# Kernel tuning notes

Measured on AMD Instinct MI355X. Metric: run time of the kernel, lower is better.

The kernel has to match this reference:

```python
import jax, jax.numpy as jnp
import numpy as np

VOCAB = 128
HID = 1024
B = 128
T = 512


def setup_inputs() -> dict:
    key = jax.random.key(0)
    ks = jax.random.split(key, 5)
    x = jax.random.randint(ks[0], (B, T), 0, VOCAB)
    Wxh = jax.random.normal(ks[1], (VOCAB, HID), dtype=jnp.float32) * 0.01
    Whh = jax.random.normal(ks[2], (HID, HID), dtype=jnp.float32) * 0.01
    bh = jnp.zeros((HID,), dtype=jnp.float32)
    # nn.Linear(hidden*2, vocab): weight [vocab, 2*hidden], bias [vocab]
    fc_w = jax.random.normal(ks[3], (VOCAB, 2 * HID), dtype=jnp.float32) * 0.02
    fc_b = jnp.zeros((VOCAB,), dtype=jnp.float32)
    return {"x": x, "Wxh": Wxh, "Whh": Whh, "bh": bh, "fc_w": fc_w, "fc_b": fc_b}


def reference(x, Wxh, Whh, bh, fc_w, fc_b):
    # one_hot(x) @ Wxh  ==  row gather from Wxh
    xe = Wxh[x]  # [B, T, H]
    h0 = jnp.zeros((x.shape[0], Whh.shape[0]), dtype=xe.dtype)

    def step(h, xt):
        h = jnp.tanh(xt + h @ Whh + bh)
        return h, h

    _, Hs = jax.lax.scan(step, h0, jnp.swapaxes(xe, 0, 1))  # [T, B, H]
    Hs = jnp.swapaxes(Hs, 0, 1)  # [B, T, H]

    # per-step full (non-causal) self-attention over hidden states, batched over t
    scores = jnp.einsum("bth,bsh->bts", Hs, Hs)          # [B, T, T]
    weights = jax.nn.softmax(scores, axis=-1)
    context = jnp.einsum("bts,bsh->bth", weights, Hs)     # [B, T, H]

    combined = jnp.concatenate([Hs, context], axis=-1)    # [B, T, 2H]
    outputs = combined @ fc_w.T + fc_b                    # [B, T, V]
    return outputs
```

## Files before the change

### kernel.cpp

```cpp
#include <hip/hip_runtime.h>
#include <cmath>

#define HID 1024
#define NB  128
#define NT  512
#define NV  128
#define NBLK 256

using u16 = unsigned short;
using u32 = unsigned int;

typedef __attribute__((ext_vector_type(8))) short s16x8;
typedef __attribute__((ext_vector_type(4))) float f32x4;

static __device__ __forceinline__ float bf2f(u16 u) {
  union { u32 i; float f; } v; v.i = ((u32)u) << 16; return v.f;
}
static __device__ __forceinline__ u16 f2bf(float f) {
  union { u32 i; float f; } v; v.f = f;
  u32 r = v.i + 0x7FFFu + ((v.i >> 16) & 1u);
  return (u16)(r >> 16);
}

__global__ __launch_bounds__(128, 1) void rnn_persist(
    const int* __restrict__ x, const float* __restrict__ Wxh,
    const float* __restrict__ Whh, const float* __restrict__ bh,
    u16* __restrict__ Hs, u32* __restrict__ ctr)
{
  const int blk  = blockIdx.x;
  const int bg   = blk & 7;
  const int cg   = blk >> 3;
  const int tid  = threadIdx.x;
  const int wave = tid >> 6;
  const int lane = tid & 63;
  const int b0   = bg * 16;
  const int c0   = cg * 32;

  __shared__ u16 Wt[32 * 1024];
  __shared__ __align__(16) u16 hstage[16 * 1024];

  for (int it = 0; it < 128; ++it) {
    int idx = tid + it * 128;
    int col = idx & 31;
    int k   = (idx >> 5) * 2;
    float w0 = Whh[(size_t)k * HID + c0 + col];
    float w1 = Whh[(size_t)(k + 1) * HID + c0 + col];
    u32 pk = ((u32)f2bf(w1) << 16) | (u32)f2bf(w0);
    u32 byteo = ((u32)col * 2048 + (u32)k * 2) ^ ((u32)(col & 7) << 4);
    *reinterpret_cast<u32*>(reinterpret_cast<char*>(Wt) + byteo) = pk;
  }

  const int frow = lane & 15;
  const int koff = (lane >> 4) * 8;
  const int col  = wave * 16 + (lane & 15);
  const int cc   = c0 + col;
  const u32 swz   = (u32)(col & 7) << 4;
  const u32 bbase = (u32)col * 2048 + (u32)koff * 2;
  const char* wtb = reinterpret_cast<const char*>(Wt);
  const char* hsb = reinterpret_cast<const char*>(hstage);
  const u32 abase = (u32)frow * 2048 + (u32)koff * 2;
  const u32 axor  = (u32)(frow & 7) << 4;

  const int srow = tid >> 3;
  const int scol = tid & 7;
  const u32 sxor = (u32)(srow & 7) << 4;
  char* sdst = reinterpret_cast<char*>(hstage) + (u32)srow * 2048;

  const float bhv = bh[cc];
  float xr[4];
  #pragma unroll
  for (int r = 0; r < 4; ++r) {
    int m = (lane >> 4) * 4 + r;
    int xt = x[(size_t)(b0 + m) * NT];
    xr[r] = Wxh[(size_t)xt * HID + cc] + bhv;
  }
  __syncthreads();

  u32* __restrict__ myctr = ctr + bg * 64;

  for (int t = 0; t < NT; ++t) {
    if (t > 0) {
      const char* src = reinterpret_cast<const char*>(
          Hs + ((size_t)(b0 + srow) * NT + (t - 1)) * HID) + scol * 16;
      uint4 s[16];
      asm volatile(
        "global_load_dwordx4 %0, %16, off sc0 sc1\n\t"
        "global_load_dwordx4 %1, %16, off offset:128 sc0 sc1\n\t"
        "global_load_dwordx4 %2, %16, off offset:256 sc0 sc1\n\t"
        "global_load_dwordx4 %3, %16, off offset:384 sc0 sc1\n\t"
        "global_load_dwordx4 %4, %16, off offset:512 sc0 sc1\n\t"
        "global_load_dwordx4 %5, %16, off offset:640 sc0 sc1\n\t"
        "global_load_dwordx4 %6, %16, off offset:768 sc0 sc1\n\t"
        "global_load_dwordx4 %7, %16, off offset:896 sc0 sc1\n\t"
        "global_load_dwordx4 %8, %16, off offset:1024 sc0 sc1\n\t"
        "global_load_dwordx4 %9, %16, off offset:1152 sc0 sc1\n\t"
        "global_load_dwordx4 %10, %16, off offset:1280 sc0 sc1\n\t"
        "global_load_dwordx4 %11, %16, off offset:1408 sc0 sc1\n\t"
        "global_load_dwordx4 %12, %16, off offset:1536 sc0 sc1\n\t"
        "global_load_dwordx4 %13, %16, off offset:1664 sc0 sc1\n\t"
        "global_load_dwordx4 %14, %16, off offset:1792 sc0 sc1\n\t"
        "global_load_dwordx4 %15, %16, off offset:1920 sc0 sc1\n\t"
        "s_waitcnt vmcnt(0)"
        : "=&v"(s[0]), "=&v"(s[1]), "=&v"(s[2]), "=&v"(s[3]),
          "=&v"(s[4]), "=&v"(s[5]), "=&v"(s[6]), "=&v"(s[7]),
          "=&v"(s[8]), "=&v"(s[9]), "=&v"(s[10]), "=&v"(s[11]),
          "=&v"(s[12]), "=&v"(s[13]), "=&v"(s[14]), "=&v"(s[15])
        : "v"(src) : "memory");
      __builtin_amdgcn_sched_barrier(0);
      #pragma unroll
      for (int j = 0; j < 16; ++j)
        *reinterpret_cast<uint4*>(sdst +
            (((u32)(scol * 16 + j * 128)) ^ sxor)) = s[j];
    }
    __syncthreads();

    f32x4 acc = {0.f, 0.f, 0.f, 0.f};
    if (t > 0) {
      #pragma unroll 8
      for (int kc = 0; kc < 32; ++kc) {
        s16x8 af = *reinterpret_cast<const s16x8*>(hsb + ((abase + (u32)kc * 64) ^ axor));
        s16x8 bf = *reinterpret_cast<const s16x8*>(wtb + ((bbase + (u32)kc * 64) ^ swz));
        acc = __builtin_amdgcn_mfma_f32_16x16x32_bf16(af, bf, acc, 0, 0, 0);
      }
    }

    #pragma unroll
    for (int r = 0; r < 4; ++r) {
      int m = (lane >> 4) * 4 + r;
      float h = tanhf(acc[r] + xr[r]);
      u16 hb = f2bf(h);
      u16* pa = Hs + ((size_t)(b0 + m) * NT + t) * HID + cc;
      asm volatile("global_store_short %0, %1, off sc0 sc1"
                   :: "v"(pa), "v"((u32)hb) : "memory");
    }
    asm volatile("s_waitcnt vmcnt(0)" ::: "memory");
    __syncthreads();

    if (tid == 0 && t < NT - 1)
      __hip_atomic_fetch_add(myctr, 1u, __ATOMIC_RELAXED, __HIP_MEMORY_SCOPE_SYSTEM);

    if (t < NT - 1) {
      #pragma unroll
      for (int r = 0; r < 4; ++r) {
        int m = (lane >> 4) * 4 + r;
        int xt = x[(size_t)(b0 + m) * NT + t + 1];
        xr[r] = Wxh[(size_t)xt * HID + cc] + bhv;
      }
      if (tid == 0) {
        const u32 target = 32u * (u32)(t + 1);
        while (__hip_atomic_load(myctr, __ATOMIC_RELAXED, __HIP_MEMORY_SCOPE_SYSTEM) < target)
          __builtin_amdgcn_s_sleep(1);
      }
    }
    __syncthreads();
  }
}

__global__ __launch_bounds__(256) void fcw_cvt(
    const float* __restrict__ fcw, u16* __restrict__ fcwb)
{
  int i = (blockIdx.x * 256 + threadIdx.x) * 4;
  float4 f = *reinterpret_cast<const float4*>(fcw + i);
  uint2 o;
  o.x = (u32)f2bf(f.x) | ((u32)f2bf(f.y) << 16);
  o.y = (u32)f2bf(f.z) | ((u32)f2bf(f.w) << 16);
  *reinterpret_cast<uint2*>(fcwb + i) = o;
}

__global__ __launch_bounds__(256) void gemm_go_mfma(
    const u16* __restrict__ Hs, const u16* __restrict__ fcwb,
    const float* __restrict__ fcb, float* __restrict__ outpre,
    u16* __restrict__ G)
{
  const int row0 = blockIdx.x * 64;
  const int w    = threadIdx.x >> 6;
  const int lane = threadIdx.x & 63;
  const int frow = lane & 15;
  const int koff = (lane >> 4) * 8;
  const int g4   = lane >> 4;

  f32x4 acc[16] = {};
  const u16* ap0 = Hs + (size_t)(row0 + w * 16 + frow) * HID + koff;

  for (int kc = 0; kc < 32; ++kc) {
    s16x8 a = *reinterpret_cast<const s16x8*>(ap0 + kc * 32);
    #pragma unroll
    for (int n = 0; n < 16; ++n) {
      int v = (n & 7) * 16 + frow;
      int kb = (n >> 3) * 1024 + kc * 32 + koff;
      s16x8 bf = *reinterpret_cast<const s16x8*>(fcwb + (size_t)v * 2048 + kb);
      acc[n] = __builtin_amdgcn_mfma_f32_16x16x32_bf16(a, bf, acc[n], 0, 0, 0);
    }
  }

  #pragma unroll
  for (int n = 0; n < 16; ++n) {
    int v = (n & 7) * 16 + frow;
    float fb = (n < 8) ? fcb[v] : 0.f;
    #pragma unroll
    for (int r = 0; r < 4; ++r) {
      size_t row = (size_t)(row0 + w * 16 + g4 * 4 + r);
      if (n < 8) outpre[row * NV + v] = acc[n][r] + fb;
      else       G[row * NV + v]      = f2bf(acc[n][r]);
    }
  }
}

__global__ __launch_bounds__(256) void attn_mfma(
    const u16* __restrict__ Hs, const u16* __restrict__ G,
    float* __restrict__ out)
{
  const int blk  = blockIdx.x;
  const int b    = blk >> 3;
  const int q0   = (blk & 7) * 64;
  const int tid  = threadIdx.x;
  const int w    = tid >> 6;
  const int lane = tid & 63;
  const int frow = lane & 15;
  const int koff = (lane >> 4) * 8;
  const int g4   = lane >> 4;

  __shared__ __align__(16) u16 Kc[64 * 128];
  __shared__ __align__(16) u16 Gt[128 * 64];
  __shared__ __align__(16) u16 Pl[64 * 64];

  const u16* __restrict__ Hb = Hs + (size_t)b * NT * HID;
  const u16* __restrict__ Gb = G  + (size_t)b * NT * NV;
  const char* kcb = reinterpret_cast<const char*>(Kc);
  const char* gtb = reinterpret_cast<const char*>(Gt);
  const char* plb = reinterpret_cast<const char*>(Pl);

  float m[4], l[4];
  #pragma unroll
  for (int r = 0; r < 4; ++r) { m[r] = -INFINITY; l[r] = 0.f; }
  f32x4 accO[8] = {};

  for (int st = 0; st < 8; ++st) {
    const int s0 = st * 64;
    __syncthreads();

    for (int it = 0; it < 32; ++it) {
      int idx = tid + it * 256;
      int s = idx >> 7, v = idx & 127;
      u16 gv = Gb[(size_t)(s0 + s) * NV + v];
      *reinterpret_cast<u16*>(const_cast<char*>(gtb) +
          (((u32)v * 128 + (u32)s * 2) ^ ((u32)(v & 7) << 4))) = gv;
    }

    f32x4 sacc[4] = {};
    for (int kc = 0; kc < 8; ++kc) {
      __syncthreads();
      #pragma unroll
      for (int i = 0; i < 4; ++i) {
        int idx = tid + i * 256;
        int row = idx >> 4, cg = idx & 15;
        uint4 kd = *reinterpret_cast<const uint4*>(
            Hb + (size_t)(s0 + row) * HID + kc * 128 + cg * 8);
        *reinterpret_cast<uint4*>(const_cast<char*>(kcb) +
            (((u32)row * 256 + (u32)cg * 16) ^ ((u32)(row & 7) << 4))) = kd;
      }
      __syncthreads();

      s16x8 aq[4];
      const u16* qp = Hb + (size_t)(q0 + w * 16 + frow) * HID + kc * 128 + koff;
      #pragma unroll
      for (int ks = 0; ks < 4; ++ks)
        aq[ks] = *reinterpret_cast<const s16x8*>(qp + ks * 32);

      #pragma unroll
      for (int ks = 0; ks < 4; ++ks) {
        #pragma unroll
        for (int n = 0; n < 4; ++n) {
          int srow = n * 16 + frow;
          s16x8 bk = *reinterpret_cast<const s16x8*>(kcb +
              (((u32)srow * 256 + (u32)(ks * 32 + koff) * 2) ^ ((u32)(srow & 7) << 4)));
          sacc[n] = __builtin_amdgcn_mfma_f32_16x16x32_bf16(aq[ks], bk, sacc[n], 0, 0, 0);
        }
      }
    }

    float p[4][4];
    float sc[4];
    #pragma unroll
    for (int r = 0; r < 4; ++r) {
      float t = fmaxf(fmaxf(sacc[0][r], sacc[1][r]), fmaxf(sacc[2][r], sacc[3][r]));
      t = fmaxf(t, __shfl_xor(t, 1));
      t = fmaxf(t, __shfl_xor(t, 2));
      t = fmaxf(t, __shfl_xor(t, 4));
      t = fmaxf(t, __shfl_xor(t, 8));
      float mn = fmaxf(m[r], t);
      sc[r] = __expf(m[r] - mn);
      float rs = 0.f;
      #pragma unroll
      for (int n = 0; n < 4; ++n) { p[n][r] = __expf(sacc[n][r] - mn); rs += p[n][r]; }
      rs += __shfl_xor(rs, 1);
      rs += __shfl_xor(rs, 2);
      rs += __shfl_xor(rs, 4);
      rs += __shfl_xor(rs, 8);
      l[r] = l[r] * sc[r] + rs;
      m[r] = mn;
    }
    #pragma unroll
    for (int v8 = 0; v8 < 8; ++v8)
      #pragma unroll
      for (int r = 0; r < 4; ++r) accO[v8][r] *= sc[r];

    #pragma unroll
    for (int n = 0; n < 4; ++n) {
      int s = n * 16 + frow;
      #pragma unroll
      for (int r = 0; r < 4; ++r) {
        int q = w * 16 + g4 * 4 + r;
        *reinterpret_cast<u16*>(const_cast<char*>(plb) +
            (((u32)q * 128 + (u32)s * 2) ^ ((u32)(q & 7) << 4))) = f2bf(p[n][r]);
      }
    }
    asm volatile("s_waitcnt lgkmcnt(0)" ::: "memory");
    __builtin_amdgcn_sched_barrier(0);

    #pragma unroll
    for (int ss = 0; ss < 2; ++ss) {
      int qrow = w * 16 + frow;
      s16x8 ap = *reinterpret_cast<const s16x8*>(plb +
          (((u32)qrow * 128 + (u32)(ss * 32 + koff) * 2) ^ ((u32)(qrow & 7) << 4)));
      #pragma unroll
      for (int v8 = 0; v8 < 8; ++v8) {
        int vrow = v8 * 16 + frow;
        s16x8 bg = *reinterpret_cast<const s16x8*>(gtb +
            (((u32)vrow * 128 + (u32)(ss * 32 + koff) * 2) ^ ((u32)(vrow & 7) << 4)));
        accO[v8] = __builtin_amdgcn_mfma_f32_16x16x32_bf16(ap, bg, accO[v8], 0, 0, 0);
      }
    }
  }

  float inv[4];
  #pragma unroll
  for (int r = 0; r < 4; ++r) inv[r] = 1.f / l[r];
  #pragma unroll
  for (int v8 = 0; v8 < 8; ++v8) {
    int c = v8 * 16 + frow;
    #pragma unroll
    for (int r = 0; r < 4; ++r) {
      size_t row = (size_t)b * NT + q0 + w * 16 + g4 * 4 + r;
      out[row * NV + c] += accO[v8][r] * inv[r];
    }
  }
}

extern "C" void kernel_launch(void* const* d_in, const int* in_sizes, int n_in,
                              void* d_out, int out_size, void* d_ws, size_t ws_size,
                              hipStream_t stream)
{
  const int*   x   = (const int*)  d_in[0];
  const float* Wxh = (const float*)d_in[1];
  const float* Whh = (const float*)d_in[2];
  const float* bh  = (const float*)d_in[3];
  const float* fcw = (const float*)d_in[4];
  const float* fcb = (const float*)d_in[5];
  float* out = (float*)d_out;

  u16* Hs   = (u16*)d_ws;
  u16* G    = Hs + (size_t)NB * NT * HID;
  u16* fcwb = G + (size_t)NB * NT * NV;
  u32* ctr  = (u32*)(fcwb + (size_t)NV * 2 * HID);

  hipMemsetAsync(ctr, 0, 8 * 64 * sizeof(u32), stream);

  rnn_persist<<<NBLK, 128, 0, stream>>>(x, Wxh, Whh, bh, Hs, ctr);

  fcw_cvt<<<256, 256, 0, stream>>>(fcw, fcwb);

  gemm_go_mfma<<<(NB * NT) / 64, 256, 0, stream>>>(Hs, fcwb, fcb, out, G);

  attn_mfma<<<NB * (NT / 64), 256, 0, stream>>>(Hs, G, out);
}
```

Baseline: 2.710 ms.

## Replace atomic counter barrier with per-block flags polled by all lanes

The per-batch-group atomic counter barrier is replaced by per-block flag words: each block stores its step number, and every wave polls the 32 peer flags directly with lanes and an __any vote, dropping the trailing __syncthreads. This removes contended atomics on one counter and the tid-0 spin followed by a block barrier from the serial per-step critical path. It also swaps tanhf for an exp/rcp-based fast tanh to shorten the elementwise tail. Risks include memory-ordering subtleties without the extra barrier and slightly reduced tanh accuracy.

```diff
diff --git a/kernel.cpp b/kernel.cpp
--- a/kernel.cpp
+++ b/kernel.cpp
@@ -21,11 +21,15 @@
   u32 r = v.i + 0x7FFFu + ((v.i >> 16) & 1u);
   return (u16)(r >> 16);
 }
+static __device__ __forceinline__ float fast_tanh(float x) {
+  float e = __expf(2.f * x);
+  return 1.f - 2.f * __builtin_amdgcn_rcpf(1.f + e);
+}
 
 __global__ __launch_bounds__(128, 1) void rnn_persist(
     const int* __restrict__ x, const float* __restrict__ Wxh,
     const float* __restrict__ Whh, const float* __restrict__ bh,
-    u16* __restrict__ Hs, u32* __restrict__ ctr)
+    u16* __restrict__ Hs, u32* __restrict__ flags)
 {
   const int blk  = blockIdx.x;
   const int bg   = blk & 7;
@@ -66,6 +70,9 @@
   const u32 sxor = (u32)(srow & 7) << 4;
   char* sdst = reinterpret_cast<char*>(hstage) + (u32)srow * 2048;
 
+  u32* flag_self = flags + (u32)bg * 1024 + (u32)cg * 32;
+  const u32* flag_poll = flags + (u32)bg * 1024 + (u32)(lane & 31) * 32;
+
   const float bhv = bh[cc];
   float xr[4];
   #pragma unroll
@@ -75,8 +82,6 @@
     xr[r] = Wxh[(size_t)xt * HID + cc] + bhv;
   }
   __syncthreads();
-
-  u32* __restrict__ myctr = ctr + bg * 64;
 
   for (int t = 0; t < NT; ++t) {
     if (t > 0) {
@@ -127,7 +132,7 @@
     #pragma unroll
     for (int r = 0; r < 4; ++r) {
       int m = (lane >> 4) * 4 + r;
-      float h = tanhf(acc[r] + xr[r]);
+      float h = fast_tanh(acc[r] + xr[r]);
       u16 hb = f2bf(h);
       u16* pa = Hs + ((size_t)(b0 + m) * NT + t) * HID + cc;
       asm volatile("global_store_short %0, %1, off sc0 sc1"
@@ -136,23 +141,25 @@
     asm volatile("s_waitcnt vmcnt(0)" ::: "memory");
     __syncthreads();
 
-    if (tid == 0 && t < NT - 1)
-      __hip_atomic_fetch_add(myctr, 1u, __ATOMIC_RELAXED, __HIP_MEMORY_SCOPE_SYSTEM);
-
     if (t < NT - 1) {
+      if (tid == 0) {
+        asm volatile("global_store_dword %0, %1, off sc0 sc1"
+                     :: "v"(flag_self), "v"((u32)(t + 1)) : "memory");
+      }
       #pragma unroll
       for (int r = 0; r < 4; ++r) {
         int m = (lane >> 4) * 4 + r;
         int xt = x[(size_t)(b0 + m) * NT + t + 1];
         xr[r] = Wxh[(size_t)xt * HID + cc] + bhv;
       }
-      if (tid == 0) {
-        const u32 target = 32u * (u32)(t + 1);
-        while (__hip_atomic_load(myctr, __ATOMIC_RELAXED, __HIP_MEMORY_SCOPE_SYSTEM) < target)
-          __builtin_amdgcn_s_sleep(1);
-      }
-    }
-    __syncthreads();
+      const u32 target = (u32)(t + 1);
+      u32 f;
+      do {
+        asm volatile("global_load_dword %0, %1, off sc0 sc1\n\t"
+                     "s_waitcnt vmcnt(0)"
+                     : "=&v"(f) : "v"(flag_poll) : "memory");
+      } while (__any((int)(f < target)));
+    }
   }
 }
 
@@ -359,14 +366,14 @@
   const float* fcb = (const float*)d_in[5];
   float* out = (float*)d_out;
 
-  u16* Hs   = (u16*)d_ws;
-  u16* G    = Hs + (size_t)NB * NT * HID;
-  u16* fcwb = G + (size_t)NB * NT * NV;
-  u32* ctr  = (u32*)(fcwb + (size_t)NV * 2 * HID);
-
-  hipMemsetAsync(ctr, 0, 8 * 64 * sizeof(u32), stream);
-
-  rnn_persist<<<NBLK, 128, 0, stream>>>(x, Wxh, Whh, bh, Hs, ctr);
+  u16* Hs    = (u16*)d_ws;
+  u16* G     = Hs + (size_t)NB * NT * HID;
+  u16* fcwb  = G + (size_t)NB * NT * NV;
+  u32* flags = (u32*)(fcwb + (size_t)NV * 2 * HID);
+
+  hipMemsetAsync(flags, 0, 8 * 1024 * sizeof(u32), stream);
+
+  rnn_persist<<<NBLK, 128, 0, stream>>>(x, Wxh, Whh, bh, Hs, flags);
 
   fcw_cvt<<<256, 256, 0, stream>>>(fcw, fcwb);
 
```

New measurement: 2.542 ms. 6.2% less time.
